# Kernel optimization log

Hardware: AMD Instinct MI355X
Metric: run time of the kernel (lower is better)

Reference implementation:

```python
import jax, jax.numpy as jnp
import numpy as np
import math

B, N, D_IN, D, D_OUT, H = 4, 2048, 128, 128, 256, 4  # D = dim_hidden//2


def _lin(key, din, dout):
    k1, k2 = jax.random.split(key)
    s = 1.0 / math.sqrt(din)
    W = jax.random.uniform(k1, (din, dout), jnp.float32, -s, s)
    b = jax.random.uniform(k2, (dout,), jnp.float32, -s, s)
    return W, b


def setup_inputs() -> dict:
    key = jax.random.key(0)
    ks = jax.random.split(key, 20)
    inp = {"X": jax.random.normal(ks[0], (B, N, D_IN), jnp.float32)}
    # mab dims: (dim_Q, dim_K) -> dim_V=D for each of the 3 MABs
    mab_dims = [(D_IN, D_IN), (D, D), (D, D)]
    ki = 1
    for i, (dq, dk) in enumerate(mab_dims):
        inp[f"m{i}_Wq"], inp[f"m{i}_bq"] = _lin(ks[ki], dq, D); ki += 1
        inp[f"m{i}_Wk"], inp[f"m{i}_bk"] = _lin(ks[ki], dk, D); ki += 1
        inp[f"m{i}_Wv"], inp[f"m{i}_bv"] = _lin(ks[ki], dk, D); ki += 1
        inp[f"m{i}_Wo"], inp[f"m{i}_bo"] = _lin(ks[ki], D, D); ki += 1
    a = math.sqrt(6.0 / (D + 1))  # xavier_uniform for S [1,1,D]
    inp["S"] = jax.random.uniform(ks[ki], (1, 1, D), jnp.float32, -a, a); ki += 1
    inp["pW"], inp["pb"] = _lin(ks[ki], D, D_OUT)
    return inp


def _mab(Q, K, Wq, bq, Wk, bk, Wv, bv, Wo, bo):
    # Linear projections
    Qp = Q @ Wq + bq                       # [B, Nq, D]
    Kp = K @ Wk + bk                       # [B, Nk, D]
    Vp = K @ Wv + bv                       # [B, Nk, D]
    b, nq, dV = Qp.shape
    dh = dV // H
    # torch split(dim_split,2)+cat(0) == head-split on last dim
    Qh = Qp.reshape(b, nq, H, dh)
    Kh = Kp.reshape(b, -1, H, dh)
    Vh = Vp.reshape(b, -1, H, dh)
    # sigmoid attention (no softmax normalizer)
    A = jax.nn.sigmoid(jnp.einsum('bnhd,bmhd->bhnm', Qh, Kh) / jnp.sqrt(jnp.float32(dV)))
    O = Qh + jnp.einsum('bhnm,bmhd->bnhd', A, Vh)
    O = O.reshape(b, nq, dV)
    # residual ReLU-FFN (no LayerNorm since ln=False)
    return O + jax.nn.relu(O @ Wo + bo)


def reference(X,
              m0_Wq, m0_bq, m0_Wk, m0_bk, m0_Wv, m0_bv, m0_Wo, m0_bo,
              m1_Wq, m1_bq, m1_Wk, m1_bk, m1_Wv, m1_bv, m1_Wo, m1_bo,
              m2_Wq, m2_bq, m2_Wk, m2_bk, m2_Wv, m2_bv, m2_Wo, m2_bo,
              S, pW, pb):
    # SAB layer 0: self-attention, dim_in -> D
    Xh = _mab(X, X, m0_Wq, m0_bq, m0_Wk, m0_bk, m0_Wv, m0_bv, m0_Wo, m0_bo)
    # SAB layer 1: D -> D
    Xh = _mab(Xh, Xh, m1_Wq, m1_bq, m1_Wk, m1_bk, m1_Wv, m1_bv, m1_Wo, m1_bo)
    # PMA pooling: seed queries attend over the set
    Sb = jnp.broadcast_to(S, (Xh.shape[0], S.shape[1], S.shape[2]))
    P = _mab(Sb, Xh, m2_Wq, m2_bq, m2_Wk, m2_bk, m2_Wv, m2_bv, m2_Wo, m2_bo)
    # final projection D -> dim_hidden
    return P @ pW + pb  # [B, num_seeds, D_OUT]
```

## Files before the change

### kernel.cpp

```cpp
#include <hip/hip_runtime.h>
#include <hip/hip_bf16.h>

typedef __hip_bfloat16 HB;
typedef __attribute__((ext_vector_type(8))) short short8;
typedef __attribute__((ext_vector_type(4))) short short4v;
typedef __attribute__((ext_vector_type(4))) float f32x4;
typedef __attribute__((ext_vector_type(2))) unsigned int uint2v;
typedef __attribute__((ext_vector_type(4))) unsigned int uint4v;

constexpr int Bn = 4, Nn = 2048, Dm = 128, Hh = 4;
constexpr int MN = Bn * Nn;
constexpr size_t SZ = (size_t)MN * Dm;

static __device__ __forceinline__ short f2bs(float x) {
    __hip_bfloat16 h = __float2bfloat16(x);
    return __builtin_bit_cast(short, h);
}
static __device__ __forceinline__ unsigned short f2bh(float x) {
    return (unsigned short)((__builtin_bit_cast(unsigned int, x) + 0x8000u) >> 16);
}
static __device__ __forceinline__ unsigned int pk2(float lo, float hi) {
    unsigned int a = __builtin_bit_cast(unsigned int, lo) + 0x8000u;
    unsigned int b = __builtin_bit_cast(unsigned int, hi) + 0x8000u;
#if __has_builtin(__builtin_amdgcn_perm)
    return __builtin_amdgcn_perm(b, a, 0x07060302u);
#else
    return (a >> 16) | (b & 0xFFFF0000u);
#endif
}

__global__ void k_wprep(const float* __restrict__ Wa, const float* __restrict__ Wb,
                        const float* __restrict__ Wc, const float* __restrict__ Wd,
                        const float* __restrict__ We, const float* __restrict__ Wf,
                        const float* __restrict__ Wg, const float* __restrict__ Wh,
                        const float* __restrict__ Wi, const float* __restrict__ Wj,
                        HB* __restrict__ WtAll) {
    const float* src;
    switch (blockIdx.x) {
        case 0: src = Wa; break; case 1: src = Wb; break;
        case 2: src = Wc; break; case 3: src = Wd; break;
        case 4: src = We; break; case 5: src = Wf; break;
        case 6: src = Wg; break; case 7: src = Wh; break;
        case 8: src = Wi; break; default: src = Wj; break;
    }
    HB* dst = WtAll + (size_t)blockIdx.x * 16384;
    #pragma unroll
    for (int it = 0; it < 2; ++it) {
        int idx = blockIdx.y * 512 + it * 256 + threadIdx.x;
        int g = idx >> 7, c = idx & 127;
        short8 p;
        #pragma unroll
        for (int j = 0; j < 8; ++j) p[j] = f2bs(src[(size_t)(g * 8 + j) * 128 + c]);
        *(short8*)((short*)dst + (size_t)idx * 8) = p;
    }
}

template<int NW, int RELU, int NEXTRA, int FUSE>
__global__ __launch_bounds__(512) void k_linm(
        const float* __restrict__ A, const float* __restrict__ extra,
        const HB* __restrict__ Wt0, const float* __restrict__ b0,
        const HB* __restrict__ Wt1, const float* __restrict__ b1,
        const HB* __restrict__ Wt2, const float* __restrict__ b2,
        float* __restrict__ C0, float* __restrict__ C1,
        HB* __restrict__ Kb, HB* __restrict__ Vt) {
    const int tid = threadIdx.x;
    const int w = tid >> 6, lane = tid & 63, l15 = lane & 15, quad = lane >> 4;
    const int row0 = blockIdx.x * 32 + (w >> 2) * 16;
    const int cbase = (w & 3) * 32;

    short8 af[4];
    #pragma unroll
    for (int kc = 0; kc < 4; ++kc) {
        const float* ap = A + (size_t)(row0 + l15) * 128 + kc * 32 + quad * 8;
        float4 x0 = *(const float4*)ap;
        float4 x1 = *(const float4*)(ap + 4);
        if (NEXTRA) {
            const float* ep = extra + (size_t)(row0 + l15) * 128 + kc * 32 + quad * 8;
            float4 e0 = *(const float4*)ep, e1 = *(const float4*)(ep + 4);
            x0.x += e0.x; x0.y += e0.y; x0.z += e0.z; x0.w += e0.w;
            x1.x += e1.x; x1.y += e1.y; x1.z += e1.z; x1.w += e1.w;
        }
        uint4v u;
        u[0] = pk2(x0.x, x0.y); u[1] = pk2(x0.z, x0.w);
        u[2] = pk2(x1.x, x1.y); u[3] = pk2(x1.z, x1.w);
        af[kc] = __builtin_bit_cast(short8, u);
    }

    f32x4 zero = {0.f, 0.f, 0.f, 0.f};
    #pragma unroll
    for (int ct = 0; ct < 2; ++ct) {
        const int col = cbase + ct * 16 + l15;
        #pragma unroll
        for (int s = 0; s < NW; ++s) {
            const HB* Wt = (s == 0) ? Wt0 : (s == 1) ? Wt1 : Wt2;
            const float* bs = (s == 0) ? b0 : (s == 1) ? b1 : b2;
            f32x4 acc = zero;
            #pragma unroll
            for (int kc = 0; kc < 4; ++kc) {
                short8 bf = *(const short8*)((const short*)Wt + ((size_t)(kc * 4 + quad) * 128 + col) * 8);
                acc = __builtin_amdgcn_mfma_f32_16x16x32_bf16(af[kc], bf, acc, 0, 0, 0);
            }
            float bb = bs[col];
            if (s == 0 || !FUSE) {
                float* Cs = (s == 0) ? C0 : C1;
                #pragma unroll
                for (int r = 0; r < 4; ++r) {
                    int row = row0 + quad * 4 + r;
                    float v = acc[r] + bb;
                    if (RELU && s == 0) {
                        float st = A[(size_t)row * 128 + col];
                        if (NEXTRA) st += extra[(size_t)row * 128 + col];
                        v = fmaxf(v, 0.f) + st;
                    }
                    Cs[(size_t)row * 128 + col] = v;
                }
            } else if (s == 1) {
                #pragma unroll
                for (int r = 0; r < 4; ++r) {
                    int row = row0 + quad * 4 + r;
                    ((unsigned short*)Kb)[(size_t)row * 128 + col] = f2bh(acc[r] + bb);
                }
            } else {
                int b_ = row0 >> 11;
                int mloc = (row0 + quad * 4) & 2047;
                int slotb = (mloc & ~31) + (((mloc & 15) >> 2) << 3) + (((mloc >> 4) & 1) << 2);
                int h_ = col >> 5, dh = col & 31;
                uint2v pv;
                pv[0] = pk2(acc[0] + bb, acc[1] + bb);
                pv[1] = pk2(acc[2] + bb, acc[3] + bb);
                *(short4v*)((short*)Vt + ((size_t)((b_ * 4 + h_) * 32 + dh)) * 2048 + slotb)
                    = __builtin_bit_cast(short4v, pv);
            }
        }
    }
}

template<int NQKV, int FUSE>
__global__ __launch_bounds__(512) void k_fused(
        const float* __restrict__ A, const float* __restrict__ extra,
        const HB* __restrict__ WtO, const float* __restrict__ bO,
        const HB* __restrict__ Wt0, const float* __restrict__ b0,
        const HB* __restrict__ Wt1, const float* __restrict__ b1,
        const HB* __restrict__ Wt2, const float* __restrict__ b2,
        float* __restrict__ C0, float* __restrict__ C1,
        HB* __restrict__ Kb, HB* __restrict__ Vt) {
    const int tid = threadIdx.x;
    const int w = tid >> 6, lane = tid & 63, l15 = lane & 15, quad = lane >> 4;
    const int lrow0 = (w >> 2) * 16;
    const int row0 = blockIdx.x * 32 + lrow0;
    const int cbase = (w & 3) * 32;

    __shared__ float xs[32 * 132];

    short8 af[4];
    #pragma unroll
    for (int kc = 0; kc < 4; ++kc) {
        const float* ap = A + (size_t)(row0 + l15) * 128 + kc * 32 + quad * 8;
        float4 x0 = *(const float4*)ap;
        float4 x1 = *(const float4*)(ap + 4);
        const float* ep = extra + (size_t)(row0 + l15) * 128 + kc * 32 + quad * 8;
        float4 e0 = *(const float4*)ep, e1 = *(const float4*)(ep + 4);
        x0.x += e0.x; x0.y += e0.y; x0.z += e0.z; x0.w += e0.w;
        x1.x += e1.x; x1.y += e1.y; x1.z += e1.z; x1.w += e1.w;
        uint4v u;
        u[0] = pk2(x0.x, x0.y); u[1] = pk2(x0.z, x0.w);
        u[2] = pk2(x1.x, x1.y); u[3] = pk2(x1.z, x1.w);
        af[kc] = __builtin_bit_cast(short8, u);
    }

    f32x4 zero = {0.f, 0.f, 0.f, 0.f};

    #pragma unroll
    for (int ct = 0; ct < 2; ++ct) {
        const int col = cbase + ct * 16 + l15;
        f32x4 acc = zero;
        #pragma unroll
        for (int kc = 0; kc < 4; ++kc) {
            short8 bf = *(const short8*)((const short*)WtO + ((size_t)(kc * 4 + quad) * 128 + col) * 8);
            acc = __builtin_amdgcn_mfma_f32_16x16x32_bf16(af[kc], bf, acc, 0, 0, 0);
        }
        float bb = bO[col];
        #pragma unroll
        for (int r = 0; r < 4; ++r) {
            int row = row0 + quad * 4 + r;
            float st = A[(size_t)row * 128 + col] + extra[(size_t)row * 128 + col];
            xs[(lrow0 + quad * 4 + r) * 132 + col] = fmaxf(acc[r] + bb, 0.f) + st;
        }
    }
    __syncthreads();

    short8 a2[4];
    {
        const float* xrow = xs + (size_t)(lrow0 + l15) * 132;
        #pragma unroll
        for (int kc = 0; kc < 4; ++kc) {
            f32x4 x0 = *(const f32x4*)(xrow + kc * 32 + quad * 8);
            f32x4 x1 = *(const f32x4*)(xrow + kc * 32 + quad * 8 + 4);
            uint4v u;
            u[0] = pk2(x0[0], x0[1]); u[1] = pk2(x0[2], x0[3]);
            u[2] = pk2(x1[0], x1[1]); u[3] = pk2(x1[2], x1[3]);
            a2[kc] = __builtin_bit_cast(short8, u);
        }
    }

    #pragma unroll
    for (int ct = 0; ct < 2; ++ct) {
        const int col = cbase + ct * 16 + l15;
        #pragma unroll
        for (int s = 0; s < NQKV; ++s) {
            const HB* Wt = (s == 0) ? Wt0 : (s == 1) ? Wt1 : Wt2;
            const float* bs = (s == 0) ? b0 : (s == 1) ? b1 : b2;
            f32x4 acc = zero;
            #pragma unroll
            for (int kc = 0; kc < 4; ++kc) {
                short8 bf = *(const short8*)((const short*)Wt + ((size_t)(kc * 4 + quad) * 128 + col) * 8);
                acc = __builtin_amdgcn_mfma_f32_16x16x32_bf16(a2[kc], bf, acc, 0, 0, 0);
            }
            float bb = bs[col];
            if (s == 0 || !FUSE) {
                float* Cs = (s == 0) ? C0 : C1;
                #pragma unroll
                for (int r = 0; r < 4; ++r) {
                    int row = row0 + quad * 4 + r;
                    Cs[(size_t)row * 128 + col] = acc[r] + bb;
                }
            } else if (s == 1) {
                #pragma unroll
                for (int r = 0; r < 4; ++r) {
                    int row = row0 + quad * 4 + r;
                    ((unsigned short*)Kb)[(size_t)row * 128 + col] = f2bh(acc[r] + bb);
                }
            } else {
                int b_ = row0 >> 11;
                int mloc = (row0 + quad * 4) & 2047;
                int slotb = (mloc & ~31) + (((mloc & 15) >> 2) << 3) + (((mloc >> 4) & 1) << 2);
                int h_ = col >> 5, dh = col & 31;
                uint2v pv;
                pv[0] = pk2(acc[0] + bb, acc[1] + bb);
                pv[1] = pk2(acc[2] + bb, acc[3] + bb);
                *(short4v*)((short*)Vt + ((size_t)((b_ * 4 + h_) * 32 + dh)) * 2048 + slotb)
                    = __builtin_bit_cast(short4v, pv);
            }
        }
    }
}

__global__ __launch_bounds__(256) void k_attn3(const float* __restrict__ Qp, const HB* __restrict__ Kbf,
                                               const HB* __restrict__ Vt, float* __restrict__ Opart) {
    const int tid = threadIdx.x;
    const int w = tid >> 6, lane = tid & 63, l15 = lane & 15, quad = lane >> 4;
    const int bh = blockIdx.x >> 6, qg = blockIdx.x & 63;
    const int b = bh >> 2, h = bh & 3;

    __shared__ float ldsacc[4][32][36];

    const float nscale = -0.08838834764831845f;

    short8 aq[2];
    #pragma unroll
    for (int qa = 0; qa < 2; ++qa) {
        const float* qp = Qp + (size_t)(b * Nn + qg * 32 + qa * 16 + l15) * 128 + h * 32 + quad * 8;
        float4 q0 = *(const float4*)qp;
        float4 q1 = *(const float4*)(qp + 4);
        uint4v u;
        u[0] = pk2(q0.x, q0.y); u[1] = pk2(q0.z, q0.w);
        u[2] = pk2(q1.x, q1.y); u[3] = pk2(q1.z, q1.w);
        aq[qa] = __builtin_bit_cast(short8, u);
    }

    f32x4 zero = {0.f, 0.f, 0.f, 0.f};
    f32x4 o[2][2];
    o[0][0] = zero; o[0][1] = zero; o[1][0] = zero; o[1][1] = zero;

    const short* Kb = (const short*)Kbf + (size_t)b * Nn * 128 + h * 32;
    const short* Vb = (const short*)Vt + (size_t)bh * 32 * Nn;

    #pragma unroll 2
    for (int m0 = w * 512; m0 < w * 512 + 512; m0 += 64) {
        short8 kb[4];
        #pragma unroll
        for (int mc = 0; mc < 4; ++mc)
            kb[mc] = *(const short8*)(Kb + (size_t)(m0 + mc * 16 + l15) * 128 + quad * 8);
        short8 vf[2][2];
        #pragma unroll
        for (int t = 0; t < 2; ++t)
            #pragma unroll
            for (int u = 0; u < 2; ++u)
                vf[t][u] = *(const short8*)(Vb + (size_t)(t * 16 + l15) * Nn + m0 + u * 32 + quad * 8);

        #pragma unroll
        for (int qa = 0; qa < 2; ++qa) {
            f32x4 s[4];
            #pragma unroll
            for (int mc = 0; mc < 4; ++mc)
                s[mc] = __builtin_amdgcn_mfma_f32_16x16x32_bf16(kb[mc], aq[qa], zero, 0, 0, 0);
            #pragma unroll
            for (int u = 0; u < 2; ++u) {
                f32x4 lo = s[2 * u], hi = s[2 * u + 1];
                float p0 = __builtin_amdgcn_rcpf(1.f + __expf(lo[0] * nscale));
                float p1 = __builtin_amdgcn_rcpf(1.f + __expf(lo[1] * nscale));
                float p2 = __builtin_amdgcn_rcpf(1.f + __expf(lo[2] * nscale));
                float p3 = __builtin_amdgcn_rcpf(1.f + __expf(lo[3] * nscale));
                float p4 = __builtin_amdgcn_rcpf(1.f + __expf(hi[0] * nscale));
                float p5 = __builtin_amdgcn_rcpf(1.f + __expf(hi[1] * nscale));
                float p6 = __builtin_amdgcn_rcpf(1.f + __expf(hi[2] * nscale));
                float p7 = __builtin_amdgcn_rcpf(1.f + __expf(hi[3] * nscale));
                uint4v pu;
                pu[0] = pk2(p0, p1); pu[1] = pk2(p2, p3);
                pu[2] = pk2(p4, p5); pu[3] = pk2(p6, p7);
                short8 pf = __builtin_bit_cast(short8, pu);
                #pragma unroll
                for (int t = 0; t < 2; ++t)
                    o[qa][t] = __builtin_amdgcn_mfma_f32_16x16x32_bf16(vf[t][u], pf, o[qa][t], 0, 0, 0);
            }
        }
    }

    #pragma unroll
    for (int qa = 0; qa < 2; ++qa)
        #pragma unroll
        for (int t = 0; t < 2; ++t)
            *(f32x4*)&ldsacc[w][qa * 16 + l15][t * 16 + quad * 4] = o[qa][t];
    __syncthreads();
    const int row = tid >> 3, cc = (tid & 7) * 4;
    f32x4 r0 = *(f32x4*)&ldsacc[0][row][cc];
    f32x4 r1 = *(f32x4*)&ldsacc[1][row][cc];
    f32x4 r2 = *(f32x4*)&ldsacc[2][row][cc];
    f32x4 r3 = *(f32x4*)&ldsacc[3][row][cc];
    f32x4 sum = (r0 + r1) + (r2 + r3);
    *(f32x4*)(Opart + (size_t)(b * Nn + qg * 32 + row) * 128 + h * 32 + cc) = sum;
}

__global__ void k_pma2(const float* __restrict__ S, const float* __restrict__ Wq, const float* __restrict__ bq,
                       const float* __restrict__ Kp, const float* __restrict__ Vp,
                       float* __restrict__ P0part) {
    const int bh = blockIdx.x, b = bh >> 2, h = bh & 3;
    const int ms = blockIdx.y;
    const int tid = threadIdx.x;
    __shared__ float4 qs4[8];
    float* qs = (float*)qs4;
    if (tid < 32) {
        float a = bq[h * 32 + tid];
        for (int k = 0; k < 128; ++k)
            a = fmaf(S[k], Wq[k * Dm + h * 32 + tid], a);
        qs[tid] = a;
    }
    __syncthreads();

    float4 q[8];
    #pragma unroll
    for (int i = 0; i < 8; ++i) q[i] = qs4[i];

    const size_t base = (size_t)b * Nn * Dm + h * 32;
    const float nscale = -0.08838834764831845f;
    const int m = ms * 256 + tid;

    const float4* kp = (const float4*)(Kp + base + (size_t)m * Dm);
    const float4* vp = (const float4*)(Vp + base + (size_t)m * Dm);
    float d0 = 0.f, d1 = 0.f, d2 = 0.f, d3 = 0.f;
    #pragma unroll
    for (int c = 0; c < 8; c += 4) {
        float4 k0 = kp[c+0], k1 = kp[c+1], k2 = kp[c+2], k3 = kp[c+3];
        d0 += q[c+0].x*k0.x + q[c+0].y*k0.y + q[c+0].z*k0.z + q[c+0].w*k0.w;
        d1 += q[c+1].x*k1.x + q[c+1].y*k1.y + q[c+1].z*k1.z + q[c+1].w*k1.w;
        d2 += q[c+2].x*k2.x + q[c+2].y*k2.y + q[c+2].z*k2.z + q[c+2].w*k2.w;
        d3 += q[c+3].x*k3.x + q[c+3].y*k3.y + q[c+3].z*k3.z + q[c+3].w*k3.w;
    }
    float dot = (d0 + d1) + (d2 + d3);
    float a = __builtin_amdgcn_rcpf(1.f + __expf(dot * nscale));
    float4 acc[8];
    #pragma unroll
    for (int c = 0; c < 8; ++c) {
        float4 vv = vp[c];
        acc[c].x = a * vv.x; acc[c].y = a * vv.y; acc[c].z = a * vv.z; acc[c].w = a * vv.w;
    }
    #pragma unroll
    for (int off = 1; off < 64; off <<= 1) {
        #pragma unroll
        for (int c = 0; c < 8; ++c) {
            acc[c].x += __shfl_xor(acc[c].x, off);
            acc[c].y += __shfl_xor(acc[c].y, off);
            acc[c].z += __shfl_xor(acc[c].z, off);
            acc[c].w += __shfl_xor(acc[c].w, off);
        }
    }
    __shared__ float red[4][32];
    const int wave = tid >> 6, lane = tid & 63;
    if (lane == 0) {
        #pragma unroll
        for (int c = 0; c < 8; ++c) {
            red[wave][c*4+0] = acc[c].x; red[wave][c*4+1] = acc[c].y;
            red[wave][c*4+2] = acc[c].z; red[wave][c*4+3] = acc[c].w;
        }
    }
    __syncthreads();
    if (tid < 32) {
        float t = (red[0][tid] + red[1][tid]) + (red[2][tid] + red[3][tid]);
        if (ms == 0) t += qs[tid];
        P0part[ms * 512 + b * 128 + h * 32 + tid] = t;
    }
}

__global__ __launch_bounds__(256) void k_tail(const float* __restrict__ P0part,
                                              const float* __restrict__ W23, const float* __restrict__ b23,
                                              const float* __restrict__ pW, const float* __restrict__ pb,
                                              float* __restrict__ out) {
    const int b = blockIdx.x, tid = threadIdx.x;
    __shared__ float staged[128], pp[128];
    if (tid < 128) {
        float s = 0.f;
        #pragma unroll
        for (int ms = 0; ms < 8; ++ms) s += P0part[ms * 512 + b * 128 + tid];
        staged[tid] = s;
    }
    __syncthreads();
    if (tid < 128) {
        float acc = b23[tid];
        #pragma unroll 8
        for (int k = 0; k < 128; ++k)
            acc = fmaf(staged[k], W23[k * 128 + tid], acc);
        pp[tid] = fmaxf(acc, 0.f) + staged[tid];
    }
    __syncthreads();
    float a = pb[tid];
    #pragma unroll 8
    for (int k = 0; k < 128; ++k)
        a = fmaf(pp[k], pW[k * 256 + tid], a);
    out[b * 256 + tid] = a;
}

extern "C" void kernel_launch(void* const* d_in, const int* in_sizes, int n_in,
                              void* d_out, int out_size, void* d_ws, size_t ws_size,
                              hipStream_t stream) {
    const float* X = (const float*)d_in[0];
    auto W = [&](int i) { return (const float*)d_in[i]; };
    float* ws = (float*)d_ws;

    float* s0 = ws + 0 * SZ;
    float* s1 = ws + 1 * SZ;
    float* s2 = ws + 2 * SZ;
    float* s3 = ws + 3 * SZ;
    HB*    Kbf = (HB*)(ws + 4 * SZ);
    HB*    Vt  = Kbf + SZ;
    HB*    WtAll = (HB*)(ws + 5 * SZ);
    auto Wt = [&](int idx) { return (const HB*)(WtAll + (size_t)idx * 16384); };
    float* P0part = s1;

    const int GLM = MN / 32;
    const int attn_blocks = Bn * Hh * (Nn / 32);
    dim3 wprep_grid(10, 4);
    dim3 pma_grid(Bn * Hh, 8);
    const float* nul = nullptr;

    k_wprep<<<wprep_grid, 256, 0, stream>>>(W(1), W(3), W(5), W(7), W(9), W(11), W(13), W(15),
                                            W(19), W(21), WtAll);

    k_linm<3,0,0,1><<<GLM, 512, 0, stream>>>(X, nul, Wt(0), W(2), Wt(1), W(4), Wt(2), W(6),
                                             s0, nullptr, Kbf, Vt);
    k_attn3<<<attn_blocks, 256, 0, stream>>>(s0, Kbf, Vt, s2);

    k_fused<3,1><<<GLM, 512, 0, stream>>>(s0, s2, Wt(3), W(8),
                                          Wt(4), W(10), Wt(5), W(12), Wt(6), W(14),
                                          s1, nullptr, Kbf, Vt);
    k_attn3<<<attn_blocks, 256, 0, stream>>>(s1, Kbf, Vt, s2);

    k_fused<2,0><<<GLM, 512, 0, stream>>>(s1, s2, Wt(7), W(16),
                                          Wt(8), W(20), Wt(9), W(22), nullptr, nul,
                                          s0, s3, nullptr, nullptr);

    k_pma2<<<pma_grid, 256, 0, stream>>>((const float*)d_in[25], W(17), W(18), s0, s3, P0part);
    k_tail<<<Bn, 256, 0, stream>>>(P0part, W(23), W(24), (const float*)d_in[26], (const float*)d_in[27],
                                   (float*)d_out);
}
```

Before: 227.5 us.

## Emit bf16 Q from projections and widen attention tiles to 64 query rows

The projection kernels now also write Q as bf16, so attention loads bf16 Q directly instead of loading fp32 and converting it. The attention kernel becomes k_attn4: 512 threads per block, 64 query rows per block, and each wave reuses its K/V fragments across four 16-row query tiles instead of two, with bh as the fast-varying block index. This is meant to cut K/V load traffic per MFMA and the Q conversion work. In exchange it uses more registers and a larger LDS reduction buffer, which lowers occupancy, and the workspace layout shifts to hold the extra Q buffer.

Result: faster. 213.5 us (-6.1%).

```diff
diff --git a/kernel.cpp b/kernel.cpp
--- a/kernel.cpp
+++ b/kernel.cpp
@@ -62,7 +62,7 @@
         const HB* __restrict__ Wt1, const float* __restrict__ b1,
         const HB* __restrict__ Wt2, const float* __restrict__ b2,
         float* __restrict__ C0, float* __restrict__ C1,
-        HB* __restrict__ Kb, HB* __restrict__ Vt) {
+        HB* __restrict__ Qb, HB* __restrict__ Kb, HB* __restrict__ Vt) {
     const int tid = threadIdx.x;
     const int w = tid >> 6, lane = tid & 63, l15 = lane & 15, quad = lane >> 4;
     const int row0 = blockIdx.x * 32 + (w >> 2) * 16;
@@ -113,6 +113,8 @@
                         v = fmaxf(v, 0.f) + st;
                     }
                     Cs[(size_t)row * 128 + col] = v;
+                    if (FUSE && s == 0)
+                        ((unsigned short*)Qb)[(size_t)row * 128 + col] = f2bh(v);
                 }
             } else if (s == 1) {
                 #pragma unroll
@@ -143,7 +145,7 @@
         const HB* __restrict__ Wt1, const float* __restrict__ b1,
         const HB* __restrict__ Wt2, const float* __restrict__ b2,
         float* __restrict__ C0, float* __restrict__ C1,
-        HB* __restrict__ Kb, HB* __restrict__ Vt) {
+        HB* __restrict__ Qb, HB* __restrict__ Kb, HB* __restrict__ Vt) {
     const int tid = threadIdx.x;
     const int w = tid >> 6, lane = tid & 63, l15 = lane & 15, quad = lane >> 4;
     const int lrow0 = (w >> 2) * 16;
@@ -222,7 +224,10 @@
                 #pragma unroll
                 for (int r = 0; r < 4; ++r) {
                     int row = row0 + quad * 4 + r;
-                    Cs[(size_t)row * 128 + col] = acc[r] + bb;
+                    float v = acc[r] + bb;
+                    Cs[(size_t)row * 128 + col] = v;
+                    if (FUSE && s == 0)
+                        ((unsigned short*)Qb)[(size_t)row * 128 + col] = f2bh(v);
                 }
             } else if (s == 1) {
                 #pragma unroll
@@ -245,38 +250,35 @@
     }
 }
 
-__global__ __launch_bounds__(256) void k_attn3(const float* __restrict__ Qp, const HB* __restrict__ Kbf,
-                                               const HB* __restrict__ Vt, float* __restrict__ Opart) {
+__global__ __launch_bounds__(512, 4) void k_attn4(const HB* __restrict__ Qb, const HB* __restrict__ Kbf,
+                                                  const HB* __restrict__ Vt, float* __restrict__ Opart) {
     const int tid = threadIdx.x;
     const int w = tid >> 6, lane = tid & 63, l15 = lane & 15, quad = lane >> 4;
-    const int bh = blockIdx.x >> 6, qg = blockIdx.x & 63;
+    const int bh = blockIdx.x & 15, qg2 = blockIdx.x >> 4;
     const int b = bh >> 2, h = bh & 3;
-
-    __shared__ float ldsacc[4][32][36];
+    const int q0row = qg2 * 64;
+
+    __shared__ float ldsacc[8][64][36];
 
     const float nscale = -0.08838834764831845f;
 
-    short8 aq[2];
-    #pragma unroll
-    for (int qa = 0; qa < 2; ++qa) {
-        const float* qp = Qp + (size_t)(b * Nn + qg * 32 + qa * 16 + l15) * 128 + h * 32 + quad * 8;
-        float4 q0 = *(const float4*)qp;
-        float4 q1 = *(const float4*)(qp + 4);
-        uint4v u;
-        u[0] = pk2(q0.x, q0.y); u[1] = pk2(q0.z, q0.w);
-        u[2] = pk2(q1.x, q1.y); u[3] = pk2(q1.z, q1.w);
-        aq[qa] = __builtin_bit_cast(short8, u);
+    short8 aq[4];
+    {
+        const short* qp = (const short*)Qb + (size_t)(b * Nn + q0row) * 128 + h * 32 + quad * 8;
+        #pragma unroll
+        for (int qa = 0; qa < 4; ++qa)
+            aq[qa] = *(const short8*)(qp + (size_t)(qa * 16 + l15) * 128);
     }
 
     f32x4 zero = {0.f, 0.f, 0.f, 0.f};
-    f32x4 o[2][2];
-    o[0][0] = zero; o[0][1] = zero; o[1][0] = zero; o[1][1] = zero;
+    f32x4 o[4][2];
+    #pragma unroll
+    for (int qa = 0; qa < 4; ++qa) { o[qa][0] = zero; o[qa][1] = zero; }
 
     const short* Kb = (const short*)Kbf + (size_t)b * Nn * 128 + h * 32;
     const short* Vb = (const short*)Vt + (size_t)bh * 32 * Nn;
 
-    #pragma unroll 2
-    for (int m0 = w * 512; m0 < w * 512 + 512; m0 += 64) {
+    for (int m0 = w * 256; m0 < w * 256 + 256; m0 += 64) {
         short8 kb[4];
         #pragma unroll
         for (int mc = 0; mc < 4; ++mc)
@@ -289,7 +291,7 @@
                 vf[t][u] = *(const short8*)(Vb + (size_t)(t * 16 + l15) * Nn + m0 + u * 32 + quad * 8);
 
         #pragma unroll
-        for (int qa = 0; qa < 2; ++qa) {
+        for (int qa = 0; qa < 4; ++qa) {
             f32x4 s[4];
             #pragma unroll
             for (int mc = 0; mc < 4; ++mc)
@@ -317,18 +319,19 @@
     }
 
     #pragma unroll
-    for (int qa = 0; qa < 2; ++qa)
+    for (int qa = 0; qa < 4; ++qa)
         #pragma unroll
         for (int t = 0; t < 2; ++t)
             *(f32x4*)&ldsacc[w][qa * 16 + l15][t * 16 + quad * 4] = o[qa][t];
     __syncthreads();
     const int row = tid >> 3, cc = (tid & 7) * 4;
-    f32x4 r0 = *(f32x4*)&ldsacc[0][row][cc];
-    f32x4 r1 = *(f32x4*)&ldsacc[1][row][cc];
-    f32x4 r2 = *(f32x4*)&ldsacc[2][row][cc];
-    f32x4 r3 = *(f32x4*)&ldsacc[3][row][cc];
-    f32x4 sum = (r0 + r1) + (r2 + r3);
-    *(f32x4*)(Opart + (size_t)(b * Nn + qg * 32 + row) * 128 + h * 32 + cc) = sum;
+    f32x4 sum = zero;
+    #pragma unroll
+    for (int ww = 0; ww < 8; ++ww) {
+        f32x4 r = *(f32x4*)&ldsacc[ww][row][cc];
+        sum += r;
+    }
+    *(f32x4*)(Opart + (size_t)(b * Nn + q0row + row) * 128 + h * 32 + cc) = sum;
 }
 
 __global__ void k_pma2(const float* __restrict__ S, const float* __restrict__ Wq, const float* __restrict__ bq,
@@ -440,14 +443,16 @@
     float* s1 = ws + 1 * SZ;
     float* s2 = ws + 2 * SZ;
     float* s3 = ws + 3 * SZ;
-    HB*    Kbf = (HB*)(ws + 4 * SZ);
-    HB*    Vt  = Kbf + SZ;
-    HB*    WtAll = (HB*)(ws + 5 * SZ);
+    HB*    B4  = (HB*)(ws + 4 * SZ);
+    HB*    Qb  = B4;
+    HB*    Kbf = B4 + SZ;
+    HB*    Vt  = B4 + 2 * SZ;
+    HB*    WtAll = B4 + 3 * SZ;
     auto Wt = [&](int idx) { return (const HB*)(WtAll + (size_t)idx * 16384); };
     float* P0part = s1;
 
     const int GLM = MN / 32;
-    const int attn_blocks = Bn * Hh * (Nn / 32);
+    const int attn_blocks = 512;
     dim3 wprep_grid(10, 4);
     dim3 pma_grid(Bn * Hh, 8);
     const float* nul = nullptr;
@@ -456,17 +461,17 @@
                                             W(19), W(21), WtAll);
 
     k_linm<3,0,0,1><<<GLM, 512, 0, stream>>>(X, nul, Wt(0), W(2), Wt(1), W(4), Wt(2), W(6),
-                                             s0, nullptr, Kbf, Vt);
-    k_attn3<<<attn_blocks, 256, 0, stream>>>(s0, Kbf, Vt, s2);
+                                             s0, nullptr, Qb, Kbf, Vt);
+    k_attn4<<<attn_blocks, 512, 0, stream>>>(Qb, Kbf, Vt, s2);
 
     k_fused<3,1><<<GLM, 512, 0, stream>>>(s0, s2, Wt(3), W(8),
                                           Wt(4), W(10), Wt(5), W(12), Wt(6), W(14),
-                                          s1, nullptr, Kbf, Vt);
-    k_attn3<<<attn_blocks, 256, 0, stream>>>(s1, Kbf, Vt, s2);
+                                          s1, nullptr, Qb, Kbf, Vt);
+    k_attn4<<<attn_blocks, 512, 0, stream>>>(Qb, Kbf, Vt, s2);
 
     k_fused<2,0><<<GLM, 512, 0, stream>>>(s1, s2, Wt(7), W(16),
                                           Wt(8), W(20), Wt(9), W(22), nullptr, nul,
-                                          s0, s3, nullptr, nullptr);
+                                          s0, s3, nullptr, nullptr, nullptr);
 
     k_pma2<<<pma_grid, 256, 0, stream>>>((const float*)d_in[25], W(17), W(18), s0, s3, P0part);
     k_tail<<<Bn, 256, 0, stream>>>(P0part, W(23), W(24), (const float*)d_in[26], (const float*)d_in[27],
```
